# Kernel optimization log

Hardware: AMD Instinct MI355X
Metric: run time of the kernel (lower is better)

The kernel has to match this reference:

```python
import jax, jax.numpy as jnp
import numpy as np

B, N, F_IN, F_OUT = 4, 512, 128, 128


def setup_inputs() -> dict:
    key = jax.random.key(0)
    k_x, k_adj, k_wm, k_wu = jax.random.split(key, 4)
    x = jax.random.normal(k_x, (B, N, F_IN), dtype=jnp.float32)
    # binary adjacency mask (dense), avg degree ~ 0.1*N
    adj = (jax.random.uniform(k_adj, (B, N, N)) < 0.1).astype(jnp.float32)
    # Linear weights stored as [in, out] (transpose of torch's [out, in])
    s_m = 1.0 / np.sqrt(2 * F_IN)
    s_u = 1.0 / np.sqrt(F_IN + F_OUT)
    W_msg = jax.random.uniform(k_wm, (2 * F_IN, F_OUT), minval=-s_m, maxval=s_m, dtype=jnp.float32)
    b_msg = jnp.zeros((F_OUT,), dtype=jnp.float32)
    W_upd = jax.random.uniform(k_wu, (F_IN + F_OUT, F_OUT), minval=-s_u, maxval=s_u, dtype=jnp.float32)
    b_upd = jnp.zeros((F_OUT,), dtype=jnp.float32)
    return {"x": x, "adj": adj, "W_msg": W_msg, "b_msg": b_msg,
            "W_upd": W_upd, "b_upd": b_upd}


def reference(x, adj, W_msg, b_msg, W_upd, b_upd):
    # Linear(cat(x_i, x_j)) == x_i @ W_i + x_j @ W_j + b  (exploit linearity to
    # avoid materializing the [B,N,N,2F] concat; math identical to torch module)
    F_in = x.shape[-1]
    Wi, Wj = W_msg[:F_in], W_msg[F_in:]
    xi = jnp.einsum('bnf,fo->bno', x, Wi)            # [B,N,out], i-term
    xj = jnp.einsum('bnf,fo->bno', x, Wj)            # [B,N,out], j-term
    # messages[b,i,j,:] = relu(xi[b,i] + xj[b,j] + b_msg); dropout is identity (eval)
    messages = jax.nn.relu(xi[:, :, None, :] + xj[:, None, :, :] + b_msg)
    # mask by adjacency and sum over j
    aggregated = jnp.einsum('bijo,bij->bio', messages, adj)  # [B,N,out]
    h_new = jnp.concatenate([x, aggregated], axis=-1)        # [B,N,F+out]
    out = jax.nn.relu(jnp.einsum('bnf,fo->bno', h_new, W_upd) + b_upd)
    return out
```

## Files before the change

### kernel.cpp

```cpp
#include <hip/hip_runtime.h>

constexpr int B_   = 4;
constexpr int N_   = 512;
constexpr int F    = 128;
constexpr int R1B  = 8;
constexpr int R2B  = 4;
constexpr int LSTW = 520;

__global__ __launch_bounds__(512, 2) void k_pre(
    const float* __restrict__ x,
    const float* __restrict__ adj,
    const float* __restrict__ Wmsg,
    const float* __restrict__ bmsg,
    const float* __restrict__ Wupd,
    float* __restrict__ xi,
    float* __restrict__ xj,
    float* __restrict__ xu,
    int*   __restrict__ lstG,
    int*   __restrict__ cntG)
{
    __shared__ __align__(16) float xs[R1B][F];
    __shared__ __align__(16) int   lst[R1B][LSTW];
    __shared__ int   cntp[R1B];
    __shared__ float ps[4][3 * R1B][F];

    const int t    = threadIdx.x;
    const int lane = t & 63;
    const int w    = t >> 6;
    const int q    = t >> 7;
    const int o    = t & 127;
    const int r0   = blockIdx.x * R1B;
    const int b    = r0 >> 9;
    const int i0   = r0 & (N_ - 1);
    const int PADJ = 2 * N_ * B_ / 2 - b * N_;

    if (blockIdx.x == 0 && t < F) xj[(size_t)(B_ * N_) * F + t] = -1e30f;

    for (int idx = t; idx < R1B * F; idx += 512)
        xs[idx >> 7][idx & 127] = x[(size_t)r0 * F + idx];

    {
        const float* arow = adj + ((size_t)b * N_ + i0 + w) * N_;
        float a[8];
        #pragma unroll
        for (int s = 0; s < 8; ++s) a[s] = arow[s * 64 + lane];
        int base = 0;
        #pragma unroll
        for (int s = 0; s < 8; ++s) {
            const unsigned long long m = __ballot(a[s] != 0.f);
            const int off = __popcll(m & ((1ull << lane) - 1ull));
            if (a[s] != 0.f) lst[w][base + off] = s * 64 + lane;
            base += __popcll(m);
        }
        const int np = (base + 7) & ~7;
        if (lane < np - base) lst[w][base + lane] = PADJ;
        if (lane == 0) cntp[w] = np;
    }
    __syncthreads();

    #pragma unroll
    for (int r = 0; r < R1B; ++r)
        for (int k = t; k < cntp[r]; k += 512)
            lstG[(size_t)(r0 + r) * LSTW + k] = lst[r][k];
    if (t < R1B) cntG[r0 + t] = cntp[t];

    float ai[R1B] = {0,0,0,0,0,0,0,0};
    float aj[R1B] = {0,0,0,0,0,0,0,0};
    float au[R1B] = {0,0,0,0,0,0,0,0};
    const int kb = q * 32;
    #pragma unroll
    for (int k = 0; k < 32; k += 4) {
        float4 xv[R1B];
        #pragma unroll
        for (int r = 0; r < R1B; ++r)
            xv[r] = *reinterpret_cast<const float4*>(&xs[r][kb + k]);
        #pragma unroll
        for (int u = 0; u < 4; ++u) {
            const int kk = kb + k + u;
            const float wi = Wmsg[(size_t)kk * F + o];
            const float wj = Wmsg[(size_t)(F + kk) * F + o];
            const float wu = Wupd[(size_t)kk * F + o];
            #pragma unroll
            for (int r = 0; r < R1B; ++r) {
                const float xk = reinterpret_cast<const float*>(&xv[r])[u];
                ai[r] = fmaf(xk, wi, ai[r]);
                aj[r] = fmaf(xk, wj, aj[r]);
                au[r] = fmaf(xk, wu, au[r]);
            }
        }
    }
    #pragma unroll
    for (int r = 0; r < R1B; ++r) {
        ps[q][r][o]            = ai[r];
        ps[q][R1B + r][o]      = aj[r];
        ps[q][2 * R1B + r][o]  = au[r];
    }
    __syncthreads();

    const float bm = bmsg[o];
    #pragma unroll
    for (int i = 0; i < 6; ++i) {
        const int v = q * 6 + i;
        float s = ps[0][v][o] + ps[1][v][o] + ps[2][v][o] + ps[3][v][o];
        float* dst = (v < R1B) ? xi : (v < 2 * R1B) ? xj : xu;
        if (v < R1B) s += bm;
        dst[(size_t)(r0 + (v & (R1B - 1))) * F + o] = s;
    }
}

__global__ __launch_bounds__(512, 2) void k_agg(
    const int*   __restrict__ lstG,
    const int*   __restrict__ cntG,
    const float* __restrict__ xi,
    const float* __restrict__ xj,
    const float* __restrict__ xu,
    const float* __restrict__ Wupd,
    const float* __restrict__ bupd,
    float* __restrict__ out)
{
    __shared__ __align__(16) int   lst[R2B][LSTW];
    __shared__ int   cntp[R2B];
    __shared__ float aggP[8][F];
    __shared__ __align__(16) float agg[R2B][F];
    __shared__ float ps[4][R2B][F];

    const int t    = threadIdx.x;
    const int lane = t & 63;
    const int w    = t >> 6;
    const int q    = t >> 7;
    const int o    = t & 127;
    const int r0   = blockIdx.x * R2B;
    const int b    = r0 >> 9;

    if (t < R2B) cntp[t] = cntG[r0 + t];
    __syncthreads();
    #pragma unroll
    for (int r = 0; r < R2B; ++r)
        for (int k = t; k < cntp[r]; k += 512)
            lst[r][k] = lstG[(size_t)(r0 + r) * LSTW + k];
    __syncthreads();

    {
        const int r = w >> 1, half = w & 1;
        const float* xjb = xj + (size_t)b * N_ * F;
        const float2 xir2 = *reinterpret_cast<const float2*>(
            &xi[(size_t)(r0 + r) * F + 2 * lane]);
        float2 acc = {0.f, 0.f};
        const int np = cntp[r];
        for (int k = half * 4; k < np; k += 8) {
            const int4 j4 = *reinterpret_cast<const int4*>(&lst[r][k]);
            const float2 v0 = *reinterpret_cast<const float2*>(&xjb[(size_t)j4.x * F + 2 * lane]);
            const float2 v1 = *reinterpret_cast<const float2*>(&xjb[(size_t)j4.y * F + 2 * lane]);
            const float2 v2 = *reinterpret_cast<const float2*>(&xjb[(size_t)j4.z * F + 2 * lane]);
            const float2 v3 = *reinterpret_cast<const float2*>(&xjb[(size_t)j4.w * F + 2 * lane]);
            acc.x += fmaxf(xir2.x + v0.x, 0.f);  acc.y += fmaxf(xir2.y + v0.y, 0.f);
            acc.x += fmaxf(xir2.x + v1.x, 0.f);  acc.y += fmaxf(xir2.y + v1.y, 0.f);
            acc.x += fmaxf(xir2.x + v2.x, 0.f);  acc.y += fmaxf(xir2.y + v2.y, 0.f);
            acc.x += fmaxf(xir2.x + v3.x, 0.f);  acc.y += fmaxf(xir2.y + v3.y, 0.f);
        }
        *reinterpret_cast<float2*>(&aggP[w][2 * lane]) = acc;
    }
    __syncthreads();
    agg[q][o] = aggP[2 * q][o] + aggP[2 * q + 1][o];
    __syncthreads();

    float res[R2B] = {0.f, 0.f, 0.f, 0.f};
    const int kb = q * 32;
    #pragma unroll
    for (int k = 0; k < 32; k += 4) {
        float4 av[R2B];
        #pragma unroll
        for (int r = 0; r < R2B; ++r)
            av[r] = *reinterpret_cast<const float4*>(&agg[r][kb + k]);
        #pragma unroll
        for (int u = 0; u < 4; ++u) {
            const float wv = Wupd[(size_t)(F + kb + k + u) * F + o];
            #pragma unroll
            for (int r = 0; r < R2B; ++r)
                res[r] = fmaf(reinterpret_cast<const float*>(&av[r])[u], wv, res[r]);
        }
    }
    #pragma unroll
    for (int r = 0; r < R2B; ++r) ps[q][r][o] = res[r];
    __syncthreads();

    if (q == 0) {
        const float bu = bupd[o];
        #pragma unroll
        for (int r = 0; r < R2B; ++r) {
            const float s = ps[0][r][o] + ps[1][r][o] + ps[2][r][o] + ps[3][r][o]
                          + xu[(size_t)(r0 + r) * F + o] + bu;
            out[(size_t)(r0 + r) * F + o] = fmaxf(s, 0.f);
        }
    }
}

extern "C" void kernel_launch(void* const* d_in, const int* in_sizes, int n_in,
                              void* d_out, int out_size, void* d_ws, size_t ws_size,
                              hipStream_t stream)
{
    const float* x    = (const float*)d_in[0];
    const float* adj  = (const float*)d_in[1];
    const float* Wmsg = (const float*)d_in[2];
    const float* bmsg = (const float*)d_in[3];
    const float* Wupd = (const float*)d_in[4];
    const float* bupd = (const float*)d_in[5];
    float* out = (float*)d_out;

    const size_t rows = (size_t)B_ * N_;
    float* xi   = (float*)d_ws;
    float* xj   = xi + rows * F;
    float* xu   = xj + (rows + 1) * F;
    int*   lstG = (int*)(xu + rows * F);
    int*   cntG = lstG + rows * LSTW;

    k_pre<<<dim3(rows / R1B), dim3(512), 0, stream>>>(
        x, adj, Wmsg, bmsg, Wupd, xi, xj, xu, lstG, cntG);
    k_agg<<<dim3(rows / R2B), dim3(512), 0, stream>>>(
        lstG, cntG, xi, xj, xu, Wupd, bupd, out);
}
```

Before: 22.00 us.

## Store xj in fp16 and restructure aggregation to one wave per row

The j-term projection is now written as half precision, which halves the bytes gathered per neighbor in the aggregation kernel. The aggregation kernel handles 8 rows per block with one wave per row instead of two. It reads the neighbor list directly from global memory with a software prefetch of the next 8 indices, so the LDS staging and partial-sum reductions are gone. The update GEMM is done with full-K per thread over two rows. Fp16 storage of xj introduces rounding error, and the padding sentinel changes to -60000 to fit the half range. Blocks are halved in number, and the prefetch reads up to 8 ints past the list end, which stays within the LSTW slack.

```diff
diff --git a/kernel.cpp b/kernel.cpp
--- a/kernel.cpp
+++ b/kernel.cpp
@@ -1,10 +1,11 @@
 #include <hip/hip_runtime.h>
+#include <hip/hip_fp16.h>
 
 constexpr int B_   = 4;
 constexpr int N_   = 512;
 constexpr int F    = 128;
 constexpr int R1B  = 8;
-constexpr int R2B  = 4;
+constexpr int R2B  = 8;
 constexpr int LSTW = 520;
 
 __global__ __launch_bounds__(512, 2) void k_pre(
@@ -13,11 +14,11 @@
     const float* __restrict__ Wmsg,
     const float* __restrict__ bmsg,
     const float* __restrict__ Wupd,
-    float* __restrict__ xi,
-    float* __restrict__ xj,
-    float* __restrict__ xu,
-    int*   __restrict__ lstG,
-    int*   __restrict__ cntG)
+    float*  __restrict__ xi,
+    __half* __restrict__ xjH,
+    float*  __restrict__ xu,
+    int*    __restrict__ lstG,
+    int*    __restrict__ cntG)
 {
     __shared__ __align__(16) float xs[R1B][F];
     __shared__ __align__(16) int   lst[R1B][LSTW];
@@ -32,9 +33,10 @@
     const int r0   = blockIdx.x * R1B;
     const int b    = r0 >> 9;
     const int i0   = r0 & (N_ - 1);
-    const int PADJ = 2 * N_ * B_ / 2 - b * N_;
-
-    if (blockIdx.x == 0 && t < F) xj[(size_t)(B_ * N_) * F + t] = -1e30f;
+    const int PADJ = B_ * N_ - b * N_;
+
+    if (blockIdx.x == 0 && t < F)
+        xjH[(size_t)(B_ * N_) * F + t] = __float2half(-60000.f);
 
     for (int idx = t; idx < R1B * F; idx += 512)
         xs[idx >> 7][idx & 127] = x[(size_t)r0 * F + idx];
@@ -91,9 +93,9 @@
     }
     #pragma unroll
     for (int r = 0; r < R1B; ++r) {
-        ps[q][r][o]            = ai[r];
-        ps[q][R1B + r][o]      = aj[r];
-        ps[q][2 * R1B + r][o]  = au[r];
+        ps[q][r][o]           = ai[r];
+        ps[q][R1B + r][o]     = aj[r];
+        ps[q][2 * R1B + r][o] = au[r];
     }
     __syncthreads();
 
@@ -101,98 +103,89 @@
     #pragma unroll
     for (int i = 0; i < 6; ++i) {
         const int v = q * 6 + i;
-        float s = ps[0][v][o] + ps[1][v][o] + ps[2][v][o] + ps[3][v][o];
-        float* dst = (v < R1B) ? xi : (v < 2 * R1B) ? xj : xu;
-        if (v < R1B) s += bm;
-        dst[(size_t)(r0 + (v & (R1B - 1))) * F + o] = s;
+        const int r = v & (R1B - 1);
+        const float s = ps[0][v][o] + ps[1][v][o] + ps[2][v][o] + ps[3][v][o];
+        if (v < R1B)            xi[(size_t)(r0 + r) * F + o] = s + bm;
+        else if (v < 2 * R1B)   xjH[(size_t)(r0 + r) * F + o] = __float2half(s);
+        else                    xu[(size_t)(r0 + r) * F + o] = s;
     }
 }
 
-__global__ __launch_bounds__(512, 2) void k_agg(
-    const int*   __restrict__ lstG,
-    const int*   __restrict__ cntG,
-    const float* __restrict__ xi,
-    const float* __restrict__ xj,
-    const float* __restrict__ xu,
-    const float* __restrict__ Wupd,
-    const float* __restrict__ bupd,
+__global__ __launch_bounds__(512) void k_agg(
+    const int*    __restrict__ lstG,
+    const int*    __restrict__ cntG,
+    const float*  __restrict__ xi,
+    const __half* __restrict__ xjH,
+    const float*  __restrict__ xu,
+    const float*  __restrict__ Wupd,
+    const float*  __restrict__ bupd,
     float* __restrict__ out)
 {
-    __shared__ __align__(16) int   lst[R2B][LSTW];
-    __shared__ int   cntp[R2B];
-    __shared__ float aggP[8][F];
     __shared__ __align__(16) float agg[R2B][F];
-    __shared__ float ps[4][R2B][F];
 
     const int t    = threadIdx.x;
     const int lane = t & 63;
     const int w    = t >> 6;
-    const int q    = t >> 7;
     const int o    = t & 127;
+    const int gg   = t >> 7;
     const int r0   = blockIdx.x * R2B;
     const int b    = r0 >> 9;
 
-    if (t < R2B) cntp[t] = cntG[r0 + t];
+    {
+        const __half* xjb = xjH + (size_t)b * N_ * F;
+        const float2 xir2 = *reinterpret_cast<const float2*>(
+            &xi[(size_t)(r0 + w) * F + 2 * lane]);
+        const int np = cntG[r0 + w];
+        const int* lrow = lstG + (size_t)(r0 + w) * LSTW;
+        float2 acc = {0.f, 0.f};
+
+        if (np > 0) {
+            int4 a = *reinterpret_cast<const int4*>(&lrow[0]);
+            int4 c = *reinterpret_cast<const int4*>(&lrow[4]);
+            for (int k = 0; k < np; k += 8) {
+                const int4 an = *reinterpret_cast<const int4*>(&lrow[k + 8]);
+                const int4 cn = *reinterpret_cast<const int4*>(&lrow[k + 12]);
+                const float2 v0 = __half22float2(*reinterpret_cast<const __half2*>(&xjb[(size_t)a.x * F + 2 * lane]));
+                const float2 v1 = __half22float2(*reinterpret_cast<const __half2*>(&xjb[(size_t)a.y * F + 2 * lane]));
+                const float2 v2 = __half22float2(*reinterpret_cast<const __half2*>(&xjb[(size_t)a.z * F + 2 * lane]));
+                const float2 v3 = __half22float2(*reinterpret_cast<const __half2*>(&xjb[(size_t)a.w * F + 2 * lane]));
+                const float2 v4 = __half22float2(*reinterpret_cast<const __half2*>(&xjb[(size_t)c.x * F + 2 * lane]));
+                const float2 v5 = __half22float2(*reinterpret_cast<const __half2*>(&xjb[(size_t)c.y * F + 2 * lane]));
+                const float2 v6 = __half22float2(*reinterpret_cast<const __half2*>(&xjb[(size_t)c.z * F + 2 * lane]));
+                const float2 v7 = __half22float2(*reinterpret_cast<const __half2*>(&xjb[(size_t)c.w * F + 2 * lane]));
+                acc.x += fmaxf(xir2.x + v0.x, 0.f);  acc.y += fmaxf(xir2.y + v0.y, 0.f);
+                acc.x += fmaxf(xir2.x + v1.x, 0.f);  acc.y += fmaxf(xir2.y + v1.y, 0.f);
+                acc.x += fmaxf(xir2.x + v2.x, 0.f);  acc.y += fmaxf(xir2.y + v2.y, 0.f);
+                acc.x += fmaxf(xir2.x + v3.x, 0.f);  acc.y += fmaxf(xir2.y + v3.y, 0.f);
+                acc.x += fmaxf(xir2.x + v4.x, 0.f);  acc.y += fmaxf(xir2.y + v4.y, 0.f);
+                acc.x += fmaxf(xir2.x + v5.x, 0.f);  acc.y += fmaxf(xir2.y + v5.y, 0.f);
+                acc.x += fmaxf(xir2.x + v6.x, 0.f);  acc.y += fmaxf(xir2.y + v6.y, 0.f);
+                acc.x += fmaxf(xir2.x + v7.x, 0.f);  acc.y += fmaxf(xir2.y + v7.y, 0.f);
+                a = an; c = cn;
+            }
+        }
+        *reinterpret_cast<float2*>(&agg[w][2 * lane]) = acc;
+    }
     __syncthreads();
-    #pragma unroll
-    for (int r = 0; r < R2B; ++r)
-        for (int k = t; k < cntp[r]; k += 512)
-            lst[r][k] = lstG[(size_t)(r0 + r) * LSTW + k];
-    __syncthreads();
-
-    {
-        const int r = w >> 1, half = w & 1;
-        const float* xjb = xj + (size_t)b * N_ * F;
-        const float2 xir2 = *reinterpret_cast<const float2*>(
-            &xi[(size_t)(r0 + r) * F + 2 * lane]);
-        float2 acc = {0.f, 0.f};
-        const int np = cntp[r];
-        for (int k = half * 4; k < np; k += 8) {
-            const int4 j4 = *reinterpret_cast<const int4*>(&lst[r][k]);
-            const float2 v0 = *reinterpret_cast<const float2*>(&xjb[(size_t)j4.x * F + 2 * lane]);
-            const float2 v1 = *reinterpret_cast<const float2*>(&xjb[(size_t)j4.y * F + 2 * lane]);
-            const float2 v2 = *reinterpret_cast<const float2*>(&xjb[(size_t)j4.z * F + 2 * lane]);
-            const float2 v3 = *reinterpret_cast<const float2*>(&xjb[(size_t)j4.w * F + 2 * lane]);
-            acc.x += fmaxf(xir2.x + v0.x, 0.f);  acc.y += fmaxf(xir2.y + v0.y, 0.f);
-            acc.x += fmaxf(xir2.x + v1.x, 0.f);  acc.y += fmaxf(xir2.y + v1.y, 0.f);
-            acc.x += fmaxf(xir2.x + v2.x, 0.f);  acc.y += fmaxf(xir2.y + v2.y, 0.f);
-            acc.x += fmaxf(xir2.x + v3.x, 0.f);  acc.y += fmaxf(xir2.y + v3.y, 0.f);
-        }
-        *reinterpret_cast<float2*>(&aggP[w][2 * lane]) = acc;
-    }
-    __syncthreads();
-    agg[q][o] = aggP[2 * q][o] + aggP[2 * q + 1][o];
-    __syncthreads();
-
-    float res[R2B] = {0.f, 0.f, 0.f, 0.f};
-    const int kb = q * 32;
-    #pragma unroll
-    for (int k = 0; k < 32; k += 4) {
-        float4 av[R2B];
-        #pragma unroll
-        for (int r = 0; r < R2B; ++r)
-            av[r] = *reinterpret_cast<const float4*>(&agg[r][kb + k]);
+
+    float res0 = 0.f, res1 = 0.f;
+    const int rA = 2 * gg, rB = 2 * gg + 1;
+    #pragma unroll
+    for (int k = 0; k < F; k += 4) {
+        const float4 a0 = *reinterpret_cast<const float4*>(&agg[rA][k]);
+        const float4 a1 = *reinterpret_cast<const float4*>(&agg[rB][k]);
         #pragma unroll
         for (int u = 0; u < 4; ++u) {
-            const float wv = Wupd[(size_t)(F + kb + k + u) * F + o];
-            #pragma unroll
-            for (int r = 0; r < R2B; ++r)
-                res[r] = fmaf(reinterpret_cast<const float*>(&av[r])[u], wv, res[r]);
-        }
-    }
-    #pragma unroll
-    for (int r = 0; r < R2B; ++r) ps[q][r][o] = res[r];
-    __syncthreads();
-
-    if (q == 0) {
-        const float bu = bupd[o];
-        #pragma unroll
-        for (int r = 0; r < R2B; ++r) {
-            const float s = ps[0][r][o] + ps[1][r][o] + ps[2][r][o] + ps[3][r][o]
-                          + xu[(size_t)(r0 + r) * F + o] + bu;
-            out[(size_t)(r0 + r) * F + o] = fmaxf(s, 0.f);
-        }
-    }
+            const float wv = Wupd[(size_t)(F + k + u) * F + o];
+            res0 = fmaf(reinterpret_cast<const float*>(&a0)[u], wv, res0);
+            res1 = fmaf(reinterpret_cast<const float*>(&a1)[u], wv, res1);
+        }
+    }
+    const float bu = bupd[o];
+    out[(size_t)(r0 + rA) * F + o] =
+        fmaxf(res0 + xu[(size_t)(r0 + rA) * F + o] + bu, 0.f);
+    out[(size_t)(r0 + rB) * F + o] =
+        fmaxf(res1 + xu[(size_t)(r0 + rB) * F + o] + bu, 0.f);
 }
 
 extern "C" void kernel_launch(void* const* d_in, const int* in_sizes, int n_in,
@@ -208,14 +201,14 @@
     float* out = (float*)d_out;
 
     const size_t rows = (size_t)B_ * N_;
-    float* xi   = (float*)d_ws;
-    float* xj   = xi + rows * F;
-    float* xu   = xj + (rows + 1) * F;
-    int*   lstG = (int*)(xu + rows * F);
-    int*   cntG = lstG + rows * LSTW;
+    float*  xi   = (float*)d_ws;
+    float*  xu   = xi + rows * F;
+    int*    lstG = (int*)(xu + rows * F);
+    int*    cntG = lstG + rows * LSTW;
+    __half* xjH  = (__half*)(cntG + rows);
 
     k_pre<<<dim3(rows / R1B), dim3(512), 0, stream>>>(
-        x, adj, Wmsg, bmsg, Wupd, xi, xj, xu, lstG, cntG);
+        x, adj, Wmsg, bmsg, Wupd, xi, xjH, xu, lstG, cntG);
     k_agg<<<dim3(rows / R2B), dim3(512), 0, stream>>>(
-        lstG, cntG, xi, xj, xu, Wupd, bupd, out);
+        lstG, cntG, xi, xjH, xu, Wupd, bupd, out);
 }
```

New measurement: 22.11 us. Within noise of the previous version (+0.5%).
